# Kernel tuning notes

Hardware: AMD Instinct MI355X
Metric: run time of the kernel (lower is better)

Reference implementation:

```python
import jax, jax.numpy as jnp
import numpy as np

B_SZ, H_DIM, W_DIM, D_MODEL = 2, 64, 64, 192
N_STATE = 16   # d_state
R_RANK = 12    # dt_rank
K_DIRS = 4
LN_EPS = 1e-5


def setup_inputs() -> dict:
    key = jax.random.key(0)
    ks = jax.random.split(key, 5)
    x = jax.random.normal(ks[0], (B_SZ, H_DIM, W_DIM, D_MODEL), jnp.float32)
    # x_proj Linear weights, small init so dt/B/C projections stay numerically tame
    x_proj_weight = jax.random.normal(ks[1], (K_DIRS, R_RANK + 2 * N_STATE, D_MODEL), jnp.float32) * 0.02
    # dt_proj weight ~ U(-rank^-0.5, rank^-0.5) as in dt_init('random')
    dt_projs_weight = jax.random.uniform(ks[2], (K_DIRS, D_MODEL, R_RANK), jnp.float32,
                                         -(R_RANK ** -0.5), R_RANK ** -0.5)
    # dt bias = inverse-softplus of dt sampled log-uniform in [1e-3, 0.1]
    dt = jnp.exp(jax.random.uniform(ks[3], (K_DIRS, D_MODEL)) * (np.log(0.1) - np.log(1e-3)) + np.log(1e-3))
    dt = jnp.clip(dt, 1e-4, None)
    dt_projs_bias = dt + jnp.log(-jnp.expm1(-dt))
    # A_log_init: log(arange(1..N)) tiled over K*D rows
    A_logs = jnp.log(jnp.tile(jnp.arange(1, N_STATE + 1, dtype=jnp.float32), (K_DIRS * D_MODEL, 1)))
    Ds = jnp.ones((K_DIRS * D_MODEL,), jnp.float32)
    ln_weight = jnp.ones((D_MODEL,), jnp.float32)
    ln_bias = jnp.zeros((D_MODEL,), jnp.float32)
    return dict(x=x, x_proj_weight=x_proj_weight, dt_projs_weight=dt_projs_weight,
                dt_projs_bias=dt_projs_bias, A_logs=A_logs, Ds=Ds,
                ln_weight=ln_weight, ln_bias=ln_bias)


def _cross_scan(x):  # x: (B, D, H, W) -> (B, 4, D, L)
    b, d, h, w = x.shape
    x0 = x.reshape(b, d, h * w)                                  # row-major scan
    x1 = jnp.transpose(x, (0, 1, 3, 2)).reshape(b, d, h * w)     # column-major scan
    xs = jnp.stack([x0, x1], axis=1)
    return jnp.concatenate([xs, jnp.flip(xs, axis=-1)], axis=1)  # + both reversed


def _cross_merge(ys, h, w):  # ys: (B, 4, D, L) -> (B, D, L)
    b, _, d, l = ys.shape
    ys = ys[:, 0:2] + jnp.flip(ys[:, 2:4], axis=-1)
    y1 = jnp.transpose(ys[:, 1].reshape(b, d, w, h), (0, 1, 3, 2)).reshape(b, d, l)
    return ys[:, 0] + y1


def _selective_scan(xs, dts, A, Bs, Cs):
    # xs, dts: (B, K, D, L); A: (K, D, N); Bs, Cs: (B, K, N, L). dts already softplus'd.
    b, k, d, l = xs.shape
    n = A.shape[-1]

    @jax.checkpoint
    def step(h_prev, t):
        x_t, dt_t, B_t, C_t = t                         # (B,K,D),(B,K,D),(B,K,N),(B,K,N)
        dA = jnp.exp(dt_t[..., None] * A)               # (B,K,D,N)
        dBx = (dt_t * x_t)[..., None] * B_t[:, :, None, :]
        h = dA * h_prev + dBx
        y = jnp.einsum('bkdn,bkn->bkd', h, C_t)
        return h, y

    seq = (jnp.moveaxis(xs, -1, 0), jnp.moveaxis(dts, -1, 0),
           jnp.moveaxis(Bs, -1, 0), jnp.moveaxis(Cs, -1, 0))
    h0 = jnp.zeros((b, k, d, n), xs.dtype)
    _, ys = jax.lax.scan(step, h0, seq)                 # ys: (L,B,K,D)
    return jnp.moveaxis(ys, 0, -1)                      # (B,K,D,L)


def reference(x, x_proj_weight, dt_projs_weight, dt_projs_bias, A_logs, Ds, ln_weight, ln_bias):
    b, h, w, d = x.shape
    l = h * w
    xc = jnp.transpose(x, (0, 3, 1, 2))                  # (B, D, H, W)
    xs = _cross_scan(xc)                                 # (B, K, D, L)
    x_dbl = jnp.einsum('bkdl,kcd->bkcl', xs, x_proj_weight)
    dts, Bs, Cs = jnp.split(x_dbl, [R_RANK, R_RANK + N_STATE], axis=2)
    dts = jnp.einsum('bkrl,kdr->bkdl', dts, dt_projs_weight)
    dts = jax.nn.softplus(dts + dt_projs_bias[None, :, :, None])   # delta_softplus + bias
    A = -jnp.exp(A_logs).reshape(K_DIRS, d, N_STATE)
    ys = _selective_scan(xs, dts, A, Bs, Cs)             # (B, K, D, L)
    ys = ys + Ds.reshape(1, K_DIRS, d, 1) * xs           # D skip connection
    y = _cross_merge(ys, h, w)                           # (B, D, L)
    y = jnp.transpose(y, (0, 2, 1))                      # (B, L, D)
    mu = jnp.mean(y, -1, keepdims=True)
    var = jnp.mean(jnp.square(y - mu), -1, keepdims=True)
    y = (y - mu) * jax.lax.rsqrt(var + LN_EPS) * ln_weight + ln_bias   # out_norm LayerNorm
    return y.reshape(b, h, w, d)
```

## Files before the change

### kernel.cpp

```cpp
#include <hip/hip_runtime.h>
#include <math.h>

#define B_SZ 2
#define HH 64
#define WW 64
#define DM 192
#define NS 16
#define RR 12
#define KD 4
#define LL (HH * WW)
#define CPROJ (RR + 2 * NS)
#define CPAD 48
#define NCH 128
#define CH (LL / NCH)
#define NBLK (B_SZ * KD * NCH)
#define KDTOT (KD * DM)
#define TLP 64
#define LOG2E 1.44269504088896340736f
#define LN2F 0.69314718055994530942f

__device__ __forceinline__ int spatial_idx(int k, int t) {
    if (k == 0) return t;
    if (k == 1) return ((t & 63) << 6) | (t >> 6);
    if (k == 2) return LL - 1 - t;
    int tp = LL - 1 - t;
    return ((tp & 63) << 6) | (tp >> 6);
}

__device__ __forceinline__ void compute_dA(float dt, const float* Avl2, bool pw, float* dA) {
    if (pw) {
        float e1 = exp2f(dt * Avl2[0]);
        dA[0] = e1;
        dA[1] = e1 * e1;
        dA[2] = dA[1] * e1;
        dA[3] = dA[1] * dA[1];
        dA[4] = dA[3] * e1;
        dA[5] = dA[3] * dA[1];
        dA[6] = dA[3] * dA[2];
        dA[7] = dA[3] * dA[3];
        dA[8] = dA[7] * e1;
        dA[9] = dA[7] * dA[1];
        dA[10] = dA[7] * dA[2];
        dA[11] = dA[7] * dA[3];
        dA[12] = dA[7] * dA[4];
        dA[13] = dA[7] * dA[5];
        dA[14] = dA[7] * dA[6];
        dA[15] = dA[7] * dA[7];
    } else {
#pragma unroll
        for (int n = 0; n < NS; ++n) dA[n] = exp2f(dt * Avl2[n]);
    }
}

__global__ __launch_bounds__(192) void prep_kernel(const float* __restrict__ dtw,
                                                   const float* __restrict__ dtb,
                                                   const float* __restrict__ Alogs,
                                                   float* __restrict__ pbuf) {
    int kd = blockIdx.x * DM + threadIdx.x;
    float* Wt  = pbuf;
    float* At  = pbuf + RR * KDTOT;
    float* bt  = At + NS * KDTOT;
    float* flg = bt + KDTOT;
#pragma unroll
    for (int r = 0; r < RR; ++r) Wt[r * KDTOT + kd] = dtw[(size_t)kd * RR + r];
    float Av[NS];
#pragma unroll
    for (int n = 0; n < NS; ++n) {
        Av[n] = -__expf(Alogs[(size_t)kd * NS + n]) * LOG2E;
        At[n * KDTOT + kd] = Av[n];
    }
    bt[kd] = dtb[kd];
    bool pws = true;
#pragma unroll
    for (int n = 0; n < NS; ++n)
        pws = pws && (fabsf(Av[n] - (float)(n + 1) * Av[0]) <= 1e-5f * fabsf(Av[n]) + 1e-30f);
    flg[kd] = pws ? 1.f : 0.f;
}

template <int PHASE>
__global__ __launch_bounds__(192) void scan_kernel(
    const float* __restrict__ x, const float* __restrict__ xdbl,
    const float* __restrict__ pbuf, const float* __restrict__ Ds,
    float* __restrict__ carry, float* __restrict__ aprod, float* __restrict__ ybuf4) {
    const int chunk = blockIdx.x & (NCH - 1);
    const int bk = blockIdx.x >> 7;
    const int k = bk & 3, b = bk >> 2;
    const int d = threadIdx.x;
    const int kd = k * DM + d;
    const int tbase = chunk * CH;

    __shared__ float xds[CH * CPAD];

    {
        float4* dst = (float4*)xds;
        const float4* src = (const float4*)(xdbl + ((size_t)bk * LL + tbase) * CPAD);
        dst[threadIdx.x] = src[threadIdx.x];
        dst[threadIdx.x + DM] = src[threadIdx.x + DM];
    }

    const float* Wt  = pbuf;
    const float* At  = pbuf + RR * KDTOT;
    const float* bt  = At + NS * KDTOT;
    const float* flg = bt + KDTOT;
    float Wdt[RR], Avl2[NS];
#pragma unroll
    for (int r = 0; r < RR; ++r) Wdt[r] = Wt[r * KDTOT + kd];
#pragma unroll
    for (int n = 0; n < NS; ++n) Avl2[n] = At[n * KDTOT + kd];
    const float bias = bt[kd];
    const bool pw = (__all(flg[kd] != 0.f ? 1 : 0) != 0);
    const float Dval = (PHASE == 3) ? Ds[kd] : 0.f;

    __syncthreads();

    const size_t cbase = ((size_t)blockIdx.x * NS) * DM + d;
    float h[NS];
    if (PHASE == 1) {
#pragma unroll
        for (int n = 0; n < NS; ++n) h[n] = 0.f;
    } else {
#pragma unroll
        for (int n = 0; n < NS; ++n) h[n] = carry[cbase + (size_t)n * DM];
    }
    float dtsum = 0.f;
    const float* xb = x + (size_t)b * LL * DM + d;
    float* yk = ybuf4 + (size_t)k * ((size_t)B_SZ * LL * DM) + (size_t)b * LL * DM + d;

    float xv_cur = xb[(size_t)spatial_idx(k, tbase) * DM];

#pragma unroll 4
    for (int tt = 0; tt < CH; ++tt) {
        int snext = spatial_idx(k, tbase + ((tt < CH - 1) ? (tt + 1) : 0));
        float xv_next = xb[(size_t)snext * DM];

        const float4* r4 = (const float4*)(xds + tt * CPAD);
        float4 q0 = r4[0], q1 = r4[1], q2 = r4[2];
        float z0 = fmaf(q0.x, Wdt[0], fmaf(q0.z, Wdt[2], fmaf(q1.x, Wdt[4],
                   fmaf(q1.z, Wdt[6], fmaf(q2.x, Wdt[8], q2.z * Wdt[10])))));
        float z1 = fmaf(q0.y, Wdt[1], fmaf(q0.w, Wdt[3], fmaf(q1.y, Wdt[5],
                   fmaf(q1.w, Wdt[7], fmaf(q2.y, Wdt[9], q2.w * Wdt[11])))));
        float z = bias + z0 + z1;
        float dt = (z > 15.f) ? z : __log2f(1.f + exp2f(z * LOG2E)) * LN2F;
        float dtx = dt * xv_cur;
        float dA[NS];
        compute_dA(dt, Avl2, pw, dA);
        if (PHASE == 1) {
            dtsum += dt;
            float4 Bq;
            Bq = r4[3];
            h[0]  = fmaf(dA[0],  h[0],  dtx * Bq.x);
            h[1]  = fmaf(dA[1],  h[1],  dtx * Bq.y);
            h[2]  = fmaf(dA[2],  h[2],  dtx * Bq.z);
            h[3]  = fmaf(dA[3],  h[3],  dtx * Bq.w);
            Bq = r4[4];
            h[4]  = fmaf(dA[4],  h[4],  dtx * Bq.x);
            h[5]  = fmaf(dA[5],  h[5],  dtx * Bq.y);
            h[6]  = fmaf(dA[6],  h[6],  dtx * Bq.z);
            h[7]  = fmaf(dA[7],  h[7],  dtx * Bq.w);
            Bq = r4[5];
            h[8]  = fmaf(dA[8],  h[8],  dtx * Bq.x);
            h[9]  = fmaf(dA[9],  h[9],  dtx * Bq.y);
            h[10] = fmaf(dA[10], h[10], dtx * Bq.z);
            h[11] = fmaf(dA[11], h[11], dtx * Bq.w);
            Bq = r4[6];
            h[12] = fmaf(dA[12], h[12], dtx * Bq.x);
            h[13] = fmaf(dA[13], h[13], dtx * Bq.y);
            h[14] = fmaf(dA[14], h[14], dtx * Bq.z);
            h[15] = fmaf(dA[15], h[15], dtx * Bq.w);
        } else {
            float y0, y1, y2, y3;
            float4 Bq, Cq;
            Bq = r4[3]; Cq = r4[7];
            h[0]  = fmaf(dA[0],  h[0],  dtx * Bq.x);  y0 = h[0] * Cq.x;
            h[1]  = fmaf(dA[1],  h[1],  dtx * Bq.y);  y1 = h[1] * Cq.y;
            h[2]  = fmaf(dA[2],  h[2],  dtx * Bq.z);  y2 = h[2] * Cq.z;
            h[3]  = fmaf(dA[3],  h[3],  dtx * Bq.w);  y3 = h[3] * Cq.w;
            Bq = r4[4]; Cq = r4[8];
            h[4]  = fmaf(dA[4],  h[4],  dtx * Bq.x);  y0 = fmaf(h[4],  Cq.x, y0);
            h[5]  = fmaf(dA[5],  h[5],  dtx * Bq.y);  y1 = fmaf(h[5],  Cq.y, y1);
            h[6]  = fmaf(dA[6],  h[6],  dtx * Bq.z);  y2 = fmaf(h[6],  Cq.z, y2);
            h[7]  = fmaf(dA[7],  h[7],  dtx * Bq.w);  y3 = fmaf(h[7],  Cq.w, y3);
            Bq = r4[5]; Cq = r4[9];
            h[8]  = fmaf(dA[8],  h[8],  dtx * Bq.x);  y0 = fmaf(h[8],  Cq.x, y0);
            h[9]  = fmaf(dA[9],  h[9],  dtx * Bq.y);  y1 = fmaf(h[9],  Cq.y, y1);
            h[10] = fmaf(dA[10], h[10], dtx * Bq.z);  y2 = fmaf(h[10], Cq.z, y2);
            h[11] = fmaf(dA[11], h[11], dtx * Bq.w);  y3 = fmaf(h[11], Cq.w, y3);
            Bq = r4[6]; Cq = r4[10];
            h[12] = fmaf(dA[12], h[12], dtx * Bq.x);  y0 = fmaf(h[12], Cq.x, y0);
            h[13] = fmaf(dA[13], h[13], dtx * Bq.y);  y1 = fmaf(h[13], Cq.y, y1);
            h[14] = fmaf(dA[14], h[14], dtx * Bq.z);  y2 = fmaf(h[14], Cq.z, y2);
            h[15] = fmaf(dA[15], h[15], dtx * Bq.w);  y3 = fmaf(h[15], Cq.w, y3);
            int scur = spatial_idx(k, tbase + tt);
            yk[(size_t)scur * DM] = (y0 + y1) + (y2 + y3) + Dval * xv_cur;
        }
        xv_cur = xv_next;
    }

    if (PHASE == 1) {
#pragma unroll
        for (int n = 0; n < NS; ++n) {
            carry[cbase + (size_t)n * DM] = h[n];
            aprod[cbase + (size_t)n * DM] = exp2f(dtsum * Avl2[n]);
        }
    }
}

__global__ __launch_bounds__(192) void fix_kernel(float* __restrict__ carry,
                                                  const float* __restrict__ aprod) {
    int idx = blockIdx.x * DM + threadIdx.x;
    int d = idx % DM;
    int r = idx / DM;
    int n = r & (NS - 1);
    int bk = r >> 4;
    size_t base = (((size_t)bk * NCH) * NS + n) * DM + d;
    const size_t stride = (size_t)NS * DM;
    float hp = 0.f;
#pragma unroll 8
    for (int c = 0; c < NCH; ++c) {
        size_t off = base + (size_t)c * stride;
        float P = aprod[off];
        float Cr = carry[off];
        carry[off] = hp;
        hp = fmaf(P, hp, Cr);
    }
}

__global__ __launch_bounds__(256) void proj_kernel(const float* __restrict__ x,
                                                   const float* __restrict__ xpw,
                                                   float* __restrict__ xdbl) {
    int blk = blockIdx.x;
    int ltile = blk % (LL / TLP);
    int bk = blk / (LL / TLP);
    int k = bk & 3;
    int b = bk >> 2;
    int l0 = ltile * TLP;

    __shared__ float xt[DM * (TLP + 1)];

    {
        int li = threadIdx.x >> 2;
        int d0 = (threadIdx.x & 3) * 48;
        int s = spatial_idx(k, l0 + li);
        const float4* xr = (const float4*)(x + ((size_t)b * LL + s) * DM + d0);
#pragma unroll
        for (int q = 0; q < 12; ++q) {
            float4 v = xr[q];
            int d = d0 + q * 4;
            xt[(d + 0) * (TLP + 1) + li] = v.x;
            xt[(d + 1) * (TLP + 1) + li] = v.y;
            xt[(d + 2) * (TLP + 1) + li] = v.z;
            xt[(d + 3) * (TLP + 1) + li] = v.w;
        }
    }
    __syncthreads();

    int lane = threadIdx.x & 63;
    int wv = threadIdx.x >> 6;
    int c0 = __builtin_amdgcn_readfirstlane(wv * 11);
    const float* wk = xpw + (size_t)k * CPROJ * DM;

    float acc[11];
#pragma unroll
    for (int ci = 0; ci < 11; ++ci) acc[ci] = 0.f;

    for (int d = 0; d < DM; ++d) {
        float xv = xt[d * (TLP + 1) + lane];
#pragma unroll
        for (int ci = 0; ci < 11; ++ci)
            acc[ci] = fmaf(xv, wk[(size_t)(c0 + ci) * DM + d], acc[ci]);
    }
    float* orow = xdbl + ((size_t)bk * LL + l0 + lane) * CPAD;
#pragma unroll
    for (int ci = 0; ci < 11; ++ci) orow[c0 + ci] = acc[ci];
}

__global__ __launch_bounds__(256) void ln_kernel(const float* __restrict__ ybuf,
                                                 const float* __restrict__ lnw,
                                                 const float* __restrict__ lnb,
                                                 float* __restrict__ out) {
    const size_t SEG = (size_t)B_SZ * LL * DM;
    int row = blockIdx.x * 4 + (threadIdx.x >> 6);
    int lane = threadIdx.x & 63;
    const float* yr = ybuf + (size_t)row * DM;
    float v0 = 0.f, v1 = 0.f, v2 = 0.f;
#pragma unroll
    for (int kq = 0; kq < KD; ++kq) {
        const float* p = yr + kq * SEG;
        v0 += p[lane];
        v1 += p[lane + 64];
        v2 += p[lane + 128];
    }
    float s = v0 + v1 + v2;
    float sq = v0 * v0 + v1 * v1 + v2 * v2;
#pragma unroll
    for (int off = 32; off >= 1; off >>= 1) {
        s += __shfl_xor(s, off, 64);
        sq += __shfl_xor(sq, off, 64);
    }
    float mu = s * (1.f / DM);
    float var = sq * (1.f / DM) - mu * mu;
    float inv = rsqrtf(var + 1e-5f);
    float* orow = out + (size_t)row * DM;
    orow[lane]       = (v0 - mu) * inv * lnw[lane]       + lnb[lane];
    orow[lane + 64]  = (v1 - mu) * inv * lnw[lane + 64]  + lnb[lane + 64];
    orow[lane + 128] = (v2 - mu) * inv * lnw[lane + 128] + lnb[lane + 128];
}

extern "C" void kernel_launch(void* const* d_in, const int* in_sizes, int n_in,
                              void* d_out, int out_size, void* d_ws, size_t ws_size,
                              hipStream_t stream) {
    const float* x    = (const float*)d_in[0];
    const float* xpw  = (const float*)d_in[1];
    const float* dtw  = (const float*)d_in[2];
    const float* dtb  = (const float*)d_in[3];
    const float* Alog = (const float*)d_in[4];
    const float* Ds   = (const float*)d_in[5];
    const float* lnw  = (const float*)d_in[6];
    const float* lnb  = (const float*)d_in[7];
    float* out = (float*)d_out;

    const size_t F_XD = (size_t)B_SZ * KD * LL * CPAD;
    const size_t F_CR = (size_t)B_SZ * KD * NCH * DM * NS;
    const size_t F_YB = (size_t)B_SZ * LL * DM;

    float* ws    = (float*)d_ws;
    float* xdbl  = ws;
    float* carry = xdbl + F_XD;
    float* aprod = carry + F_CR;
    float* ybuf4 = aprod + F_CR;
    float* pbuf  = ybuf4 + 4 * F_YB;

    prep_kernel<<<KDTOT / DM, DM, 0, stream>>>(dtw, dtb, Alog, pbuf);
    proj_kernel<<<B_SZ * KD * (LL / TLP), 256, 0, stream>>>(x, xpw, xdbl);
    scan_kernel<1><<<NBLK, DM, 0, stream>>>(x, xdbl, pbuf, Ds, carry, aprod, ybuf4);
    fix_kernel<<<128, DM, 0, stream>>>(carry, aprod);
    scan_kernel<3><<<NBLK, DM, 0, stream>>>(x, xdbl, pbuf, Ds, carry, aprod, ybuf4);
    ln_kernel<<<(B_SZ * LL) / 4, 256, 0, stream>>>(ybuf4, lnw, lnb, out);
}
```

Before: 107.2 us.

## Interleave two independent scan sub-chunks per thread and recompute chunk decay in fix

Each scan thread now carries two independent 16-step chunks (A and B) of its 32-step block and advances them in lockstep. This doubles instruction-level parallelism on the serial recurrence and halves the sequential depth per thread. The carry-propagation stage now has 256 chunks instead of 128. The per-chunk decay product array is replaced by a stored dt-sum per chunk and d, and fix_kernel recomputes exp2 from it, which removes a 16x-larger buffer. The costs are twice the register state, and a fix loop that is twice as long and does exp2 in its serial chain.

```diff
diff --git a/kernel.cpp b/kernel.cpp
--- a/kernel.cpp
+++ b/kernel.cpp
@@ -11,9 +11,10 @@
 #define LL (HH * WW)
 #define CPROJ (RR + 2 * NS)
 #define CPAD 48
-#define NCH 128
-#define CH (LL / NCH)
-#define NBLK (B_SZ * KD * NCH)
+#define NCH 256
+#define CH 16
+#define QBLK 128
+#define NBLK (B_SZ * KD * QBLK)
 #define KDTOT (KD * DM)
 #define TLP 64
 #define LOG2E 1.44269504088896340736f
@@ -52,6 +53,73 @@
     }
 }
 
+template <int PHASE>
+__device__ __forceinline__ float do_step(const float* row, const float* Wdt, float bias,
+                                         const float* Avl2, bool pw, float xv,
+                                         float* h, float& dtsum) {
+    const float4* r4 = (const float4*)row;
+    float4 q0 = r4[0], q1 = r4[1], q2 = r4[2];
+    float z0 = fmaf(q0.x, Wdt[0], fmaf(q0.z, Wdt[2], fmaf(q1.x, Wdt[4],
+               fmaf(q1.z, Wdt[6], fmaf(q2.x, Wdt[8], q2.z * Wdt[10])))));
+    float z1 = fmaf(q0.y, Wdt[1], fmaf(q0.w, Wdt[3], fmaf(q1.y, Wdt[5],
+               fmaf(q1.w, Wdt[7], fmaf(q2.y, Wdt[9], q2.w * Wdt[11])))));
+    float z = bias + z0 + z1;
+    float dt = (z > 15.f) ? z : __log2f(1.f + exp2f(z * LOG2E)) * LN2F;
+    float dtx = dt * xv;
+    float dA[NS];
+    compute_dA(dt, Avl2, pw, dA);
+    float y = 0.f;
+    if (PHASE == 1) {
+        dtsum += dt;
+        float4 Bq;
+        Bq = r4[3];
+        h[0]  = fmaf(dA[0],  h[0],  dtx * Bq.x);
+        h[1]  = fmaf(dA[1],  h[1],  dtx * Bq.y);
+        h[2]  = fmaf(dA[2],  h[2],  dtx * Bq.z);
+        h[3]  = fmaf(dA[3],  h[3],  dtx * Bq.w);
+        Bq = r4[4];
+        h[4]  = fmaf(dA[4],  h[4],  dtx * Bq.x);
+        h[5]  = fmaf(dA[5],  h[5],  dtx * Bq.y);
+        h[6]  = fmaf(dA[6],  h[6],  dtx * Bq.z);
+        h[7]  = fmaf(dA[7],  h[7],  dtx * Bq.w);
+        Bq = r4[5];
+        h[8]  = fmaf(dA[8],  h[8],  dtx * Bq.x);
+        h[9]  = fmaf(dA[9],  h[9],  dtx * Bq.y);
+        h[10] = fmaf(dA[10], h[10], dtx * Bq.z);
+        h[11] = fmaf(dA[11], h[11], dtx * Bq.w);
+        Bq = r4[6];
+        h[12] = fmaf(dA[12], h[12], dtx * Bq.x);
+        h[13] = fmaf(dA[13], h[13], dtx * Bq.y);
+        h[14] = fmaf(dA[14], h[14], dtx * Bq.z);
+        h[15] = fmaf(dA[15], h[15], dtx * Bq.w);
+    } else {
+        float y0, y1, y2, y3;
+        float4 Bq, Cq;
+        Bq = r4[3]; Cq = r4[7];
+        h[0]  = fmaf(dA[0],  h[0],  dtx * Bq.x);  y0 = h[0] * Cq.x;
+        h[1]  = fmaf(dA[1],  h[1],  dtx * Bq.y);  y1 = h[1] * Cq.y;
+        h[2]  = fmaf(dA[2],  h[2],  dtx * Bq.z);  y2 = h[2] * Cq.z;
+        h[3]  = fmaf(dA[3],  h[3],  dtx * Bq.w);  y3 = h[3] * Cq.w;
+        Bq = r4[4]; Cq = r4[8];
+        h[4]  = fmaf(dA[4],  h[4],  dtx * Bq.x);  y0 = fmaf(h[4],  Cq.x, y0);
+        h[5]  = fmaf(dA[5],  h[5],  dtx * Bq.y);  y1 = fmaf(h[5],  Cq.y, y1);
+        h[6]  = fmaf(dA[6],  h[6],  dtx * Bq.z);  y2 = fmaf(h[6],  Cq.z, y2);
+        h[7]  = fmaf(dA[7],  h[7],  dtx * Bq.w);  y3 = fmaf(h[7],  Cq.w, y3);
+        Bq = r4[5]; Cq = r4[9];
+        h[8]  = fmaf(dA[8],  h[8],  dtx * Bq.x);  y0 = fmaf(h[8],  Cq.x, y0);
+        h[9]  = fmaf(dA[9],  h[9],  dtx * Bq.y);  y1 = fmaf(h[9],  Cq.y, y1);
+        h[10] = fmaf(dA[10], h[10], dtx * Bq.z);  y2 = fmaf(h[10], Cq.z, y2);
+        h[11] = fmaf(dA[11], h[11], dtx * Bq.w);  y3 = fmaf(h[11], Cq.w, y3);
+        Bq = r4[6]; Cq = r4[10];
+        h[12] = fmaf(dA[12], h[12], dtx * Bq.x);  y0 = fmaf(h[12], Cq.x, y0);
+        h[13] = fmaf(dA[13], h[13], dtx * Bq.y);  y1 = fmaf(h[13], Cq.y, y1);
+        h[14] = fmaf(dA[14], h[14], dtx * Bq.z);  y2 = fmaf(h[14], Cq.z, y2);
+        h[15] = fmaf(dA[15], h[15], dtx * Bq.w);  y3 = fmaf(h[15], Cq.w, y3);
+        y = (y0 + y1) + (y2 + y3);
+    }
+    return y;
+}
+
 __global__ __launch_bounds__(192) void prep_kernel(const float* __restrict__ dtw,
                                                    const float* __restrict__ dtb,
                                                    const float* __restrict__ Alogs,
@@ -81,15 +149,15 @@
 __global__ __launch_bounds__(192) void scan_kernel(
     const float* __restrict__ x, const float* __restrict__ xdbl,
     const float* __restrict__ pbuf, const float* __restrict__ Ds,
-    float* __restrict__ carry, float* __restrict__ aprod, float* __restrict__ ybuf4) {
-    const int chunk = blockIdx.x & (NCH - 1);
+    float* __restrict__ carry, float* __restrict__ dtsumb, float* __restrict__ ybuf4) {
+    const int q = blockIdx.x & (QBLK - 1);
     const int bk = blockIdx.x >> 7;
     const int k = bk & 3, b = bk >> 2;
     const int d = threadIdx.x;
     const int kd = k * DM + d;
-    const int tbase = chunk * CH;
-
-    __shared__ float xds[CH * CPAD];
+    const int tbase = q * 32;
+
+    __shared__ float xds[32 * CPAD];
 
     {
         float4* dst = (float4*)xds;
@@ -113,112 +181,67 @@
 
     __syncthreads();
 
-    const size_t cbase = ((size_t)blockIdx.x * NS) * DM + d;
-    float h[NS];
+    const size_t cbA = ((size_t)(bk * NCH + 2 * q) * NS) * DM + d;
+    const size_t cbB = cbA + (size_t)NS * DM;
+    float hA[NS], hB[NS];
     if (PHASE == 1) {
 #pragma unroll
-        for (int n = 0; n < NS; ++n) h[n] = 0.f;
+        for (int n = 0; n < NS; ++n) { hA[n] = 0.f; hB[n] = 0.f; }
     } else {
 #pragma unroll
-        for (int n = 0; n < NS; ++n) h[n] = carry[cbase + (size_t)n * DM];
-    }
-    float dtsum = 0.f;
+        for (int n = 0; n < NS; ++n) {
+            hA[n] = carry[cbA + (size_t)n * DM];
+            hB[n] = carry[cbB + (size_t)n * DM];
+        }
+    }
+    float dtsA = 0.f, dtsB = 0.f;
     const float* xb = x + (size_t)b * LL * DM + d;
     float* yk = ybuf4 + (size_t)k * ((size_t)B_SZ * LL * DM) + (size_t)b * LL * DM + d;
 
-    float xv_cur = xb[(size_t)spatial_idx(k, tbase) * DM];
-
 #pragma unroll 4
     for (int tt = 0; tt < CH; ++tt) {
-        int snext = spatial_idx(k, tbase + ((tt < CH - 1) ? (tt + 1) : 0));
-        float xv_next = xb[(size_t)snext * DM];
-
-        const float4* r4 = (const float4*)(xds + tt * CPAD);
-        float4 q0 = r4[0], q1 = r4[1], q2 = r4[2];
-        float z0 = fmaf(q0.x, Wdt[0], fmaf(q0.z, Wdt[2], fmaf(q1.x, Wdt[4],
-                   fmaf(q1.z, Wdt[6], fmaf(q2.x, Wdt[8], q2.z * Wdt[10])))));
-        float z1 = fmaf(q0.y, Wdt[1], fmaf(q0.w, Wdt[3], fmaf(q1.y, Wdt[5],
-                   fmaf(q1.w, Wdt[7], fmaf(q2.y, Wdt[9], q2.w * Wdt[11])))));
-        float z = bias + z0 + z1;
-        float dt = (z > 15.f) ? z : __log2f(1.f + exp2f(z * LOG2E)) * LN2F;
-        float dtx = dt * xv_cur;
-        float dA[NS];
-        compute_dA(dt, Avl2, pw, dA);
-        if (PHASE == 1) {
-            dtsum += dt;
-            float4 Bq;
-            Bq = r4[3];
-            h[0]  = fmaf(dA[0],  h[0],  dtx * Bq.x);
-            h[1]  = fmaf(dA[1],  h[1],  dtx * Bq.y);
-            h[2]  = fmaf(dA[2],  h[2],  dtx * Bq.z);
-            h[3]  = fmaf(dA[3],  h[3],  dtx * Bq.w);
-            Bq = r4[4];
-            h[4]  = fmaf(dA[4],  h[4],  dtx * Bq.x);
-            h[5]  = fmaf(dA[5],  h[5],  dtx * Bq.y);
-            h[6]  = fmaf(dA[6],  h[6],  dtx * Bq.z);
-            h[7]  = fmaf(dA[7],  h[7],  dtx * Bq.w);
-            Bq = r4[5];
-            h[8]  = fmaf(dA[8],  h[8],  dtx * Bq.x);
-            h[9]  = fmaf(dA[9],  h[9],  dtx * Bq.y);
-            h[10] = fmaf(dA[10], h[10], dtx * Bq.z);
-            h[11] = fmaf(dA[11], h[11], dtx * Bq.w);
-            Bq = r4[6];
-            h[12] = fmaf(dA[12], h[12], dtx * Bq.x);
-            h[13] = fmaf(dA[13], h[13], dtx * Bq.y);
-            h[14] = fmaf(dA[14], h[14], dtx * Bq.z);
-            h[15] = fmaf(dA[15], h[15], dtx * Bq.w);
-        } else {
-            float y0, y1, y2, y3;
-            float4 Bq, Cq;
-            Bq = r4[3]; Cq = r4[7];
-            h[0]  = fmaf(dA[0],  h[0],  dtx * Bq.x);  y0 = h[0] * Cq.x;
-            h[1]  = fmaf(dA[1],  h[1],  dtx * Bq.y);  y1 = h[1] * Cq.y;
-            h[2]  = fmaf(dA[2],  h[2],  dtx * Bq.z);  y2 = h[2] * Cq.z;
-            h[3]  = fmaf(dA[3],  h[3],  dtx * Bq.w);  y3 = h[3] * Cq.w;
-            Bq = r4[4]; Cq = r4[8];
-            h[4]  = fmaf(dA[4],  h[4],  dtx * Bq.x);  y0 = fmaf(h[4],  Cq.x, y0);
-            h[5]  = fmaf(dA[5],  h[5],  dtx * Bq.y);  y1 = fmaf(h[5],  Cq.y, y1);
-            h[6]  = fmaf(dA[6],  h[6],  dtx * Bq.z);  y2 = fmaf(h[6],  Cq.z, y2);
-            h[7]  = fmaf(dA[7],  h[7],  dtx * Bq.w);  y3 = fmaf(h[7],  Cq.w, y3);
-            Bq = r4[5]; Cq = r4[9];
-            h[8]  = fmaf(dA[8],  h[8],  dtx * Bq.x);  y0 = fmaf(h[8],  Cq.x, y0);
-            h[9]  = fmaf(dA[9],  h[9],  dtx * Bq.y);  y1 = fmaf(h[9],  Cq.y, y1);
-            h[10] = fmaf(dA[10], h[10], dtx * Bq.z);  y2 = fmaf(h[10], Cq.z, y2);
-            h[11] = fmaf(dA[11], h[11], dtx * Bq.w);  y3 = fmaf(h[11], Cq.w, y3);
-            Bq = r4[6]; Cq = r4[10];
-            h[12] = fmaf(dA[12], h[12], dtx * Bq.x);  y0 = fmaf(h[12], Cq.x, y0);
-            h[13] = fmaf(dA[13], h[13], dtx * Bq.y);  y1 = fmaf(h[13], Cq.y, y1);
-            h[14] = fmaf(dA[14], h[14], dtx * Bq.z);  y2 = fmaf(h[14], Cq.z, y2);
-            h[15] = fmaf(dA[15], h[15], dtx * Bq.w);  y3 = fmaf(h[15], Cq.w, y3);
-            int scur = spatial_idx(k, tbase + tt);
-            yk[(size_t)scur * DM] = (y0 + y1) + (y2 + y3) + Dval * xv_cur;
+        int sA = spatial_idx(k, tbase + tt);
+        int sB = spatial_idx(k, tbase + 16 + tt);
+        float xvA = xb[(size_t)sA * DM];
+        float xvB = xb[(size_t)sB * DM];
+        float yA = do_step<PHASE>(xds + tt * CPAD,        Wdt, bias, Avl2, pw, xvA, hA, dtsA);
+        float yB = do_step<PHASE>(xds + (16 + tt) * CPAD, Wdt, bias, Avl2, pw, xvB, hB, dtsB);
+        if (PHASE == 3) {
+            yk[(size_t)sA * DM] = yA + Dval * xvA;
+            yk[(size_t)sB * DM] = yB + Dval * xvB;
         }
-        xv_cur = xv_next;
     }
 
     if (PHASE == 1) {
 #pragma unroll
         for (int n = 0; n < NS; ++n) {
-            carry[cbase + (size_t)n * DM] = h[n];
-            aprod[cbase + (size_t)n * DM] = exp2f(dtsum * Avl2[n]);
+            carry[cbA + (size_t)n * DM] = hA[n];
+            carry[cbB + (size_t)n * DM] = hB[n];
         }
-    }
-}
-
-__global__ __launch_bounds__(192) void fix_kernel(float* __restrict__ carry,
-                                                  const float* __restrict__ aprod) {
+        size_t db = (size_t)(bk * NCH + 2 * q) * DM + d;
+        dtsumb[db] = dtsA;
+        dtsumb[db + DM] = dtsB;
+    }
+}
+
+__global__ __launch_bounds__(192) void fix_kernel(const float* __restrict__ pbuf,
+                                                  float* __restrict__ carry,
+                                                  const float* __restrict__ dtsumb) {
     int idx = blockIdx.x * DM + threadIdx.x;
     int d = idx % DM;
     int r = idx / DM;
     int n = r & (NS - 1);
     int bk = r >> 4;
-    size_t base = (((size_t)bk * NCH) * NS + n) * DM + d;
+    const float* At = pbuf + RR * KDTOT;
+    float Av = At[n * KDTOT + (bk & 3) * DM + d];
+    size_t cb = ((size_t)bk * NCH * NS + n) * DM + d;
+    size_t db = (size_t)bk * NCH * DM + d;
     const size_t stride = (size_t)NS * DM;
     float hp = 0.f;
 #pragma unroll 8
     for (int c = 0; c < NCH; ++c) {
-        size_t off = base + (size_t)c * stride;
-        float P = aprod[off];
+        float P = exp2f(dtsumb[db + (size_t)c * DM] * Av);
+        size_t off = cb + (size_t)c * stride;
         float Cr = carry[off];
         carry[off] = hp;
         hp = fmaf(P, hp, Cr);
@@ -320,20 +343,21 @@
     float* out = (float*)d_out;
 
     const size_t F_XD = (size_t)B_SZ * KD * LL * CPAD;
-    const size_t F_CR = (size_t)B_SZ * KD * NCH * DM * NS;
+    const size_t F_CR = (size_t)B_SZ * KD * NCH * NS * DM;
+    const size_t F_DS = (size_t)B_SZ * KD * NCH * DM;
     const size_t F_YB = (size_t)B_SZ * LL * DM;
 
-    float* ws    = (float*)d_ws;
-    float* xdbl  = ws;
-    float* carry = xdbl + F_XD;
-    float* aprod = carry + F_CR;
-    float* ybuf4 = aprod + F_CR;
-    float* pbuf  = ybuf4 + 4 * F_YB;
+    float* ws     = (float*)d_ws;
+    float* xdbl   = ws;
+    float* carry  = xdbl + F_XD;
+    float* dtsumb = carry + F_CR;
+    float* ybuf4  = dtsumb + F_DS;
+    float* pbuf   = ybuf4 + 4 * F_YB;
 
     prep_kernel<<<KDTOT / DM, DM, 0, stream>>>(dtw, dtb, Alog, pbuf);
     proj_kernel<<<B_SZ * KD * (LL / TLP), 256, 0, stream>>>(x, xpw, xdbl);
-    scan_kernel<1><<<NBLK, DM, 0, stream>>>(x, xdbl, pbuf, Ds, carry, aprod, ybuf4);
-    fix_kernel<<<128, DM, 0, stream>>>(carry, aprod);
-    scan_kernel<3><<<NBLK, DM, 0, stream>>>(x, xdbl, pbuf, Ds, carry, aprod, ybuf4);
+    scan_kernel<1><<<NBLK, DM, 0, stream>>>(x, xdbl, pbuf, Ds, carry, dtsumb, ybuf4);
+    fix_kernel<<<128, DM, 0, stream>>>(pbuf, carry, dtsumb);
+    scan_kernel<3><<<NBLK, DM, 0, stream>>>(x, xdbl, pbuf, Ds, carry, dtsumb, ybuf4);
     ln_kernel<<<(B_SZ * LL) / 4, 256, 0, stream>>>(ybuf4, lnw, lnb, out);
 }
```

Result: slower. 129.9 us (+21.2%).
